# Kernel optimization log

Hardware: AMD Instinct MI355X
Metric: run time of the kernel (lower is better)

Reference implementation:

```python
import jax, jax.numpy as jnp
import numpy as np
from jax import lax

DN = ('NCHW', 'OIHW', 'NCHW')


def _conv_block(x, w, g, b, pool):
    # 3x3 conv (pad 1), BN-inference folded to affine (g, b), ReLU, optional 2x2 maxpool
    x = lax.conv_general_dilated(x, w, (1, 1), 'SAME', dimension_numbers=DN)
    x = jax.nn.relu(x * g[None, :, None, None] + b[None, :, None, None])
    if pool:
        x = lax.reduce_window(x, -jnp.inf, lax.max, (1, 1, 2, 2), (1, 1, 2, 2), 'VALID')
    return x


def _encode(x, w1, g1, b1, w2, g2, b2, w3, g3, b3, w4, g4, b4):
    # Conv64F: pool in blocks 1,2 (84->42->21), no pool in blocks 3,4; then global avg pool
    x = _conv_block(x, w1, g1, b1, True)
    x = _conv_block(x, w2, g2, b2, True)
    x = _conv_block(x, w3, g3, b3, False)
    x = _conv_block(x, w4, g4, b4, False)
    return jnp.mean(x, axis=(2, 3))  # (N, 64)


def setup_inputs() -> dict:
    key = jax.random.key(0)
    ks = jax.random.split(key, 9)
    B, NQ, Way, Shot, C, H, W = 4, 15, 5, 5, 3, 84, 84
    d = {
        'query': jax.random.normal(ks[0], (B, NQ, C, H, W), jnp.float32),
        'support': jax.random.normal(ks[1], (B, Way, Shot, C, H, W), jnp.float32),
        'w1': jax.random.normal(ks[2], (64, 3, 3, 3), jnp.float32) * 0.1,
        'g1': jnp.ones((64,), jnp.float32), 'b1': jnp.zeros((64,), jnp.float32),
        'w2': jax.random.normal(ks[3], (64, 64, 3, 3), jnp.float32) * 0.05,
        'g2': jnp.ones((64,), jnp.float32), 'b2': jnp.zeros((64,), jnp.float32),
        'w3': jax.random.normal(ks[4], (64, 64, 3, 3), jnp.float32) * 0.05,
        'g3': jnp.ones((64,), jnp.float32), 'b3': jnp.zeros((64,), jnp.float32),
        'w4': jax.random.normal(ks[5], (64, 64, 3, 3), jnp.float32) * 0.05,
        'g4': jnp.ones((64,), jnp.float32), 'b4': jnp.zeros((64,), jnp.float32),
        'fc1_w': jax.random.normal(ks[6], (64, 64), jnp.float32) * 0.1,
        'fc1_b': jnp.zeros((64,), jnp.float32),
        'fc2_w': jax.random.normal(ks[7], (32, 64), jnp.float32) * 0.1,
        'fc2_b': jnp.zeros((32,), jnp.float32),
        'fc3_w': jax.random.normal(ks[8], (1, 32), jnp.float32) * 0.1,
        'fc3_b': jnp.zeros((1,), jnp.float32),
    }
    return d


def reference(query, support, w1, g1, b1, w2, g2, b2, w3, g3, b3, w4, g4, b4,
              fc1_w, fc1_b, fc2_w, fc2_b, fc3_w, fc3_b):
    B, NQ, C, H, W = query.shape
    _, Way, Shot = support.shape[:3]
    enc = lambda x: _encode(x, w1, g1, b1, w2, g2, b2, w3, g3, b3, w4, g4, b4)
    q_emb = enc(query.reshape(-1, C, H, W)).reshape(B, NQ, 64)
    s_emb = enc(support.reshape(-1, C, H, W)).reshape(B, Way, Shot, 64)
    # batched pairwise |diff|: (B, NQ, Way, Shot, 64)
    diff = jnp.abs(q_emb[:, :, None, None, :] - s_emb[:, None, :, :, :])
    # relation net (dropout is identity at inference)
    h = jax.nn.relu(jnp.einsum('bqwsd,od->bqwso', diff, fc1_w) + fc1_b)
    h = jax.nn.relu(jnp.einsum('bqwsd,od->bqwso', h, fc2_w) + fc2_b)
    sim = jax.nn.sigmoid(jnp.einsum('bqwsd,od->bqwso', h, fc3_w) + fc3_b)[..., 0]
    scores = jnp.mean(sim, axis=3)  # mean over Shot -> (B, NQ, Way)
    return scores.reshape(B * NQ, Way)
```

## Files before the change

kernel.cpp:

```cpp
#include <hip/hip_runtime.h>
#include <math.h>

typedef unsigned short ushort_t;
typedef __attribute__((ext_vector_type(8))) short bf16x8;
typedef __attribute__((ext_vector_type(16))) float f32x16;

__device__ __forceinline__ ushort_t f2bf(float f) {
    unsigned u = __float_as_uint(f);
    u += 0x7fffu + ((u >> 16) & 1u);
    return (ushort_t)(u >> 16);
}
__device__ __forceinline__ float bf2f(ushort_t h) {
    return __uint_as_float(((unsigned)h) << 16);
}

template <int HP>
__device__ __forceinline__ void zero_halo(ushort_t* buf, int n, int t, int nthr)
{
    const size_t PSTR = (size_t)160 * HP * HP * 32;
    constexpr int W = HP - 2;
    constexpr int NB = 2 * HP + 2 * W;
    for (int j = t; j < 2 * NB; j += nthr) {
        const int pl = j / NB, i = j % NB;
        int yy, xx;
        if (i < HP)            { yy = 0;            xx = i; }
        else if (i < 2 * HP)   { yy = HP - 1;       xx = i - HP; }
        else if (i < 2*HP + W) { yy = i - 2*HP + 1; xx = 0; }
        else                   { yy = i - 2*HP - W + 1; xx = HP - 1; }
        uint4* p = (uint4*)(buf + pl * PSTR +
                            ((size_t)n * HP * HP + yy * HP + xx) * 32);
        const uint4 z = make_uint4(0u, 0u, 0u, 0u);
        p[0] = z; p[1] = z;
    }
}

__global__ __launch_bounds__(256) void prep_k(
    const float* __restrict__ q, const float* __restrict__ s,
    const float* __restrict__ w1, const float* __restrict__ w2,
    const float* __restrict__ w3, const float* __restrict__ w4,
    ushort_t* __restrict__ p0, ushort_t* __restrict__ pw1,
    ushort_t* __restrict__ pw234,
    ushort_t* __restrict__ P1, ushort_t* __restrict__ P2,
    ushort_t* __restrict__ P3, float* __restrict__ embv)
{
    const int b = blockIdx.x, t = threadIdx.x;
    if (b < 160) {
        const int n = b;
        const float* src; int nn;
        if (n < 60) { src = q; nn = n; } else { src = s; nn = n - 60; }
        const float* img = src + (size_t)nn * 3 * 7056;
        for (int px = t; px < 7396; px += 256) {
            const int y = px / 86, x = px % 86;
            uint4 v = make_uint4(0u, 0u, 0u, 0u);
            if (y >= 1 && y <= 84 && x >= 1 && x <= 84) {
                const int o = (y - 1) * 84 + (x - 1);
                const unsigned c0 = f2bf(img[o]);
                const unsigned c1 = f2bf(img[7056 + o]);
                const unsigned c2 = f2bf(img[14112 + o]);
                v.x = c0 | (c1 << 16);
                v.y = c2;
            }
            *(uint4*)(p0 + ((size_t)n * 7396 + px) * 8) = v;
        }
    } else if (b < 167) {
        const int bw = b - 160;
        if (bw == 0) {
            for (int idx = t; idx < 5120; idx += 256) {
                const int sl = idx >> 10, rem = idx & 1023;
                const int co = rem >> 4, c = rem & 15;
                const int h = c >> 3, e = c & 7, tap = 2 * sl + h;
                float v = 0.f;
                if (tap < 9 && e < 3) v = w1[co * 27 + e * 9 + tap];
                pw1[idx] = f2bf(v);
            }
        } else {
            const int l = (bw - 1) >> 1, pass = (bw - 1) & 1;
            const float* w = (l == 0) ? w2 : (l == 1) ? w3 : w4;
            ushort_t* dst = pw234 + l * 36864 + pass * 18432;
            for (int idx = t; idx < 18432; idx += 256) {
                const int c  = idx & 7;
                const int co = (idx >> 3) & 63;
                const int h  = (idx >> 9) & 1;
                const int kl = (idx >> 10) & 1;
                const int tap = idx >> 11;
                const int ci = pass * 32 + kl * 16 + h * 8 + c;
                dst[idx] = f2bf(w[co * 576 + ci * 9 + tap]);
            }
        }
    } else if (b < 327) {
        const int n = b - 167;
        zero_halo<44>(P1, n, t, 256);
        zero_halo<23>(P2, n, t, 256);
        zero_halo<23>(P3, n, t, 256);
    } else {
        for (int i = t; i < 2560; i += 256)
            ((uint4*)embv)[i] = make_uint4(0u, 0u, 0u, 0u);
    }
}

__global__ __launch_bounds__(256, 2) void conv1_lds_k(
    const ushort_t* __restrict__ p0, const ushort_t* __restrict__ pw1,
    const float* __restrict__ gg, const float* __restrict__ bb,
    ushort_t* __restrict__ outp)
{
    constexpr int ROWB = 86 * 16 + 16;
    constexpr int R = 6;
    constexpr int PXB = 84;
    constexpr size_t PLANE1 = (size_t)160 * 1936 * 32;

    __shared__ __align__(16) char alds[R * ROWB];
    __shared__ __align__(16) char blds[10240];

    const int tid = threadIdx.x, wv = tid >> 6, lane = tid & 63;
    const int l31 = lane & 31, h = lane >> 5;
    const int s = blockIdx.x, n = blockIdx.y;
    const int row0 = 4 * s;

    int abase[3];
#pragma unroll
    for (int t = 0; t < 3; ++t) {
        const int ml = wv * 96 + t * 32 + l31;
        int pp = ml >> 2; if (pp > PXB - 1) pp = PXB - 1;
        const int qd = ml & 3;
        const int p = PXB * s + pp;
        const int pr = p / 42, pc = p % 42;
        const int yl = 2 * (pr - 2 * s) + (qd >> 1);
        const int xl = 2 * pc + (qd & 1);
        abase[t] = yl * ROWB + xl * 16;
    }
    int boff[2];
#pragma unroll
    for (int nt = 0; nt < 2; ++nt) boff[nt] = (nt * 32 + l31) * 32 + h * 16;

    {
        const uint4* src = (const uint4*)(p0 + (size_t)n * 7396 * 8);
        for (int i = tid; i < R * 86; i += 256) {
            const int y = i / 86, x = i - y * 86;
            *(uint4*)(alds + y * ROWB + x * 16) = src[(row0 + y) * 86 + x];
        }
    }
    for (int i = tid; i < 640; i += 256)
        ((uint4*)blds)[i] = ((const uint4*)pw1)[i];

    f32x16 acc[3][2];
#pragma unroll
    for (int t = 0; t < 3; ++t)
#pragma unroll
        for (int nt = 0; nt < 2; ++nt)
#pragma unroll
            for (int r = 0; r < 16; ++r) acc[t][nt][r] = 0.f;

    __syncthreads();

#pragma unroll
    for (int st = 0; st < 5; ++st) {
        int tap = 2 * st + h;
        if (tap > 8) tap = 8;
        const int imm = (tap / 3) * ROWB + (tap % 3) * 16;
        const bf16x8 a0 = *(const bf16x8*)(alds + abase[0] + imm);
        const bf16x8 a1 = *(const bf16x8*)(alds + abase[1] + imm);
        const bf16x8 a2 = *(const bf16x8*)(alds + abase[2] + imm);
#pragma unroll
        for (int nt = 0; nt < 2; ++nt) {
            const bf16x8 b = *(const bf16x8*)(blds + st * 2048 + boff[nt]);
            acc[0][nt] = __builtin_amdgcn_mfma_f32_32x32x16_bf16(
                a0, b, acc[0][nt], 0, 0, 0);
            acc[1][nt] = __builtin_amdgcn_mfma_f32_32x32x16_bf16(
                a1, b, acc[1][nt], 0, 0, 0);
            acc[2][nt] = __builtin_amdgcn_mfma_f32_32x32x16_bf16(
                a2, b, acc[2][nt], 0, 0, 0);
        }
    }

    float gv2[2], bv2[2];
#pragma unroll
    for (int nt = 0; nt < 2; ++nt) {
        gv2[nt] = gg[nt * 32 + l31];
        bv2[nt] = bb[nt * 32 + l31];
    }
#pragma unroll
    for (int t = 0; t < 3; ++t) {
#pragma unroll
        for (int g = 0; g < 4; ++g) {
            const int mbase = wv * 96 + t * 32 + 8 * g + 4 * h;
            const int pp = mbase >> 2;
            if (pp >= PXB) continue;
            const int p = PXB * s + pp;
            const int pr = p / 42, pc = p % 42;
            ushort_t* dpix =
                outp + ((size_t)n * 1936 + (pr + 1) * 44 + (pc + 1)) * 32 + l31;
#pragma unroll
            for (int nt = 0; nt < 2; ++nt) {
                float mx = 0.f;
#pragma unroll
                for (int qd = 0; qd < 4; ++qd)
                    mx = fmaxf(mx, fmaf(acc[t][nt][4 * g + qd], gv2[nt], bv2[nt]));
                dpix[nt * PLANE1] = f2bf(mx);
            }
        }
    }
}

template <int HINP, int POOL, int EPI, int RPB, int WAVES>
__device__ __forceinline__ void conv_body(
    const ushort_t* __restrict__ act, const ushort_t* __restrict__ pkw,
    const float* __restrict__ gg, const float* __restrict__ bb,
    ushort_t* __restrict__ outp)
{
    constexpr int MT   = 2;
    constexpr int NTHR = WAVES * 64;
    constexpr int PXB  = 21 * RPB;
    constexpr int R    = POOL ? 2 * RPB + 2 : RPB + 2;
    constexpr int ROWB = HINP * 80;
    const size_t APLANE = (size_t)160 * HINP * HINP * 32;
    constexpr size_t OPLANE = (size_t)160 * 529 * 32;

    __shared__ __align__(16) char alds[R * ROWB];

    const int tid = threadIdx.x, wv = tid >> 6, lane = tid & 63;
    const int l31 = lane & 31, h = lane >> 5;
    const int s = blockIdx.x, n = blockIdx.y;

    const int row0 = POOL ? 2 * RPB * s : RPB * s;

    int abase[MT];
#pragma unroll
    for (int t = 0; t < MT; ++t) {
        const int ml = wv * (MT * 32) + t * 32 + l31;
        int yl, xl;
        if (POOL) {
            int pp = ml >> 2; if (pp > PXB - 1) pp = PXB - 1;
            int p = PXB * s + pp; if (p > 440) p = 440;
            const int qd = ml & 3;
            yl = 2 * (p / 21 - RPB * s) + (qd >> 1);
            xl = 2 * (p % 21) + (qd & 1);
        } else {
            int pp = ml; if (pp > PXB - 1) pp = PXB - 1;
            int p = PXB * s + pp; if (p > 440) p = 440;
            yl = p / 21 - RPB * s;
            xl = p % 21;
        }
        abase[t] = yl * ROWB + xl * 80 + h * 16;
    }
    int boff[2];
#pragma unroll
    for (int nt = 0; nt < 2; ++nt) boff[nt] = h * 1024 + (nt * 32 + l31) * 16;

    f32x16 acc[MT][2];
#pragma unroll
    for (int t = 0; t < MT; ++t)
#pragma unroll
        for (int nt = 0; nt < 2; ++nt)
#pragma unroll
            for (int r = 0; r < 16; ++r) acc[t][nt][r] = 0.f;

    bf16x8 br[4][2];

#define B_LD(S, SLOT)                                                      \
    {                                                                      \
        br[SLOT][0] = *(const bf16x8*)(bg + (S)*2048 + boff[0]);           \
        br[SLOT][1] = *(const bf16x8*)(bg + (S)*2048 + boff[1]);           \
    }

    for (int ph = 0; ph < 2; ++ph) {
        const char* bg = (const char*)pkw + ph * 36864;
        B_LD(0, 0) B_LD(1, 1) B_LD(2, 2) B_LD(3, 3)

        if (ph) __syncthreads();
        {
            const uint4* src = (const uint4*)(act +
                (ph * APLANE + (size_t)n * HINP * HINP * 32));
            for (int p = tid; p < R * HINP; p += NTHR) {
                const int y = p / HINP, x = p - y * HINP;
                const int row = min(row0 + y, HINP - 1);
                const uint4* sp = src + ((size_t)row * HINP + x) * 4;
                const uint4 c0 = sp[0], c1 = sp[1], c2 = sp[2], c3 = sp[3];
                char* d = alds + y * ROWB + x * 80;
                *(uint4*)(d)      = c0;
                *(uint4*)(d + 16) = c1;
                *(uint4*)(d + 32) = c2;
                *(uint4*)(d + 48) = c3;
            }
        }
        __syncthreads();

#pragma unroll
        for (int st = 0; st < 18; ++st) {
            const int sl = st & 3;
            const int tap = st >> 1, kl = st & 1;
            const int imm = (tap / 3) * ROWB + (tap % 3) * 80 + kl * 32;
            const bf16x8 a0 = *(const bf16x8*)(alds + abase[0] + imm);
            const bf16x8 a1 = *(const bf16x8*)(alds + abase[1] + imm);
            const bf16x8 b0 = br[sl][0];
            const bf16x8 b1 = br[sl][1];
            if (st < 14) B_LD(st + 4, sl)
            acc[0][0] = __builtin_amdgcn_mfma_f32_32x32x16_bf16(
                a0, b0, acc[0][0], 0, 0, 0);
            acc[1][0] = __builtin_amdgcn_mfma_f32_32x32x16_bf16(
                a1, b0, acc[1][0], 0, 0, 0);
            acc[0][1] = __builtin_amdgcn_mfma_f32_32x32x16_bf16(
                a0, b1, acc[0][1], 0, 0, 0);
            acc[1][1] = __builtin_amdgcn_mfma_f32_32x32x16_bf16(
                a1, b1, acc[1][1], 0, 0, 0);
        }
    }
#undef B_LD

    float gv2[2], bv2[2];
#pragma unroll
    for (int nt = 0; nt < 2; ++nt) {
        gv2[nt] = gg[nt * 32 + l31];
        bv2[nt] = bb[nt * 32 + l31];
    }

    if (EPI == 0) {
#pragma unroll
        for (int t = 0; t < MT; ++t) {
#pragma unroll
            for (int g = 0; g < 4; ++g) {
                const int mbase = wv * (MT * 32) + t * 32 + 8 * g + 4 * h;
                const int pp = mbase >> 2;
                const int p_img = PXB * s + pp;
                if (pp >= PXB || p_img >= 441) continue;
                const int py = p_img / 21, px = p_img % 21;
                ushort_t* dpix = outp +
                    ((size_t)n * 529 + (py + 1) * 23 + (px + 1)) * 32 + l31;
#pragma unroll
                for (int nt = 0; nt < 2; ++nt) {
                    float mx = 0.f;
#pragma unroll
                    for (int qd = 0; qd < 4; ++qd)
                        mx = fmaxf(mx,
                                   fmaf(acc[t][nt][4 * g + qd], gv2[nt], bv2[nt]));
                    dpix[nt * OPLANE] = f2bf(mx);
                }
            }
        }
    } else if (EPI == 1) {
#pragma unroll
        for (int t = 0; t < MT; ++t) {
#pragma unroll
            for (int r = 0; r < 16; ++r) {
                const int mloc = wv * (MT * 32) + t * 32 +
                                 (r & 3) + 8 * (r >> 2) + 4 * h;
                const int m_img = PXB * s + mloc;
                if (mloc >= PXB || m_img >= 441) continue;
                const int y = m_img / 21, x = m_img % 21;
#pragma unroll
                for (int nt = 0; nt < 2; ++nt) {
                    const float v =
                        fmaxf(fmaf(acc[t][nt][r], gv2[nt], bv2[nt]), 0.f);
                    outp[nt * OPLANE +
                         ((size_t)n * 529 + (y + 1) * 23 + (x + 1)) * 32 + l31] =
                        f2bf(v);
                }
            }
        }
    } else {
        float* embf = (float*)outp;
#pragma unroll
        for (int nt = 0; nt < 2; ++nt) {
            float sum = 0.f;
#pragma unroll
            for (int t = 0; t < MT; ++t) {
#pragma unroll
                for (int r = 0; r < 16; ++r) {
                    const int mloc = wv * (MT * 32) + t * 32 +
                                     (r & 3) + 8 * (r >> 2) + 4 * h;
                    const int m_img = PXB * s + mloc;
                    if (mloc < PXB && m_img < 441)
                        sum += fmaxf(fmaf(acc[t][nt][r], gv2[nt], bv2[nt]), 0.f);
                }
            }
            atomicAdd(&embf[(size_t)n * 64 + nt * 32 + l31],
                      sum * (1.f / 441.f));
        }
    }
}

__global__ __launch_bounds__(256, 4) void conv2_k(
    const ushort_t* __restrict__ act, const ushort_t* __restrict__ pkw,
    const float* __restrict__ gg, const float* __restrict__ bb,
    ushort_t* __restrict__ outp)
{ conv_body<44, 1, 0, 3, 4>(act, pkw, gg, bb, outp); }

__global__ __launch_bounds__(128, 3) void conv3_k(
    const ushort_t* __restrict__ act, const ushort_t* __restrict__ pkw,
    const float* __restrict__ gg, const float* __restrict__ bb,
    ushort_t* __restrict__ outp)
{ conv_body<23, 0, 1, 6, 2>(act, pkw, gg, bb, outp); }

__global__ __launch_bounds__(128, 3) void conv4_k(
    const ushort_t* __restrict__ act, const ushort_t* __restrict__ pkw,
    const float* __restrict__ gg, const float* __restrict__ bb,
    ushort_t* __restrict__ outp)
{ conv_body<23, 0, 2, 6, 2>(act, pkw, gg, bb, outp); }

__global__ __launch_bounds__(64) void relation_k(
    const float* __restrict__ emb,
    const float* __restrict__ fc1w, const float* __restrict__ fc1b,
    const float* __restrict__ fc2w, const float* __restrict__ fc2b,
    const float* __restrict__ fc3w, const float* __restrict__ fc3b,
    float* __restrict__ out)
{
    const int idx = blockIdx.x;
    const int w = idx % 5;
    const int bq = idx / 5;
    const int b = bq / 15;
    const int t = threadIdx.x;

    __shared__ float dif[64], h1v[64], h2v[32];
    const float qv = emb[(size_t)bq * 64 + t];

    float ssum = 0.f;
    for (int s = 0; s < 5; ++s) {
        const int simg = 60 + ((b * 5 + w) * 5 + s);
        __syncthreads();
        dif[t] = fabsf(qv - emb[(size_t)simg * 64 + t]);
        __syncthreads();
        float a = fc1b[t];
        for (int d = 0; d < 64; ++d) a = fmaf(fc1w[t * 64 + d], dif[d], a);
        a = fmaxf(a, 0.f);
        __syncthreads();
        h1v[t] = a;
        __syncthreads();
        if (t < 32) {
            float h = fc2b[t];
            for (int d = 0; d < 64; ++d) h = fmaf(fc2w[t * 64 + d], h1v[d], h);
            h2v[t] = fmaxf(h, 0.f);
        }
        __syncthreads();
        float p = (t < 32) ? fc3w[t] * h2v[t] : 0.f;
#pragma unroll
        for (int off = 32; off > 0; off >>= 1) p += __shfl_down(p, off);
        if (t == 0) {
            const float z = p + fc3b[0];
            ssum += 1.f / (1.f + expf(-z));
        }
    }
    if (t == 0) out[idx] = ssum * 0.2f;
}

extern "C" void kernel_launch(void* const* d_in, const int* in_sizes, int n_in,
                              void* d_out, int out_size, void* d_ws, size_t ws_size,
                              hipStream_t stream)
{
    const float* q    = (const float*)d_in[0];
    const float* s    = (const float*)d_in[1];
    const float* w1   = (const float*)d_in[2];
    const float* g1   = (const float*)d_in[3];
    const float* b1p  = (const float*)d_in[4];
    const float* w2   = (const float*)d_in[5];
    const float* g2   = (const float*)d_in[6];
    const float* b2p  = (const float*)d_in[7];
    const float* w3   = (const float*)d_in[8];
    const float* g3   = (const float*)d_in[9];
    const float* b3p  = (const float*)d_in[10];
    const float* w4   = (const float*)d_in[11];
    const float* g4   = (const float*)d_in[12];
    const float* b4p  = (const float*)d_in[13];
    const float* fc1w = (const float*)d_in[14];
    const float* fc1b = (const float*)d_in[15];
    const float* fc2w = (const float*)d_in[16];
    const float* fc2b = (const float*)d_in[17];
    const float* fc3w = (const float*)d_in[18];
    const float* fc3b = (const float*)d_in[19];
    float* out = (float*)d_out;

    char* ws = (char*)d_ws;
    ushort_t* P0    = (ushort_t*)(ws + 0);
    ushort_t* P1    = (ushort_t*)(ws + 18933760);
    ushort_t* P2    = (ushort_t*)(ws + 58583040);
    ushort_t* P3    = (ushort_t*)(ws + 69416960);
    float*    embv  = (float*)   (ws + 80250880);
    ushort_t* pw1   = (ushort_t*)(ws + 80291840);
    ushort_t* pw234 = (ushort_t*)(ws + 80302080);

    prep_k<<<dim3(328), 256, 0, stream>>>(q, s, w1, w2, w3, w4,
                                          P0, pw1, pw234, P1, P2, P3, embv);

    conv1_lds_k<<<dim3(21, 160), 256, 0, stream>>>(P0, pw1, g1, b1p, P1);

    conv2_k<<<dim3(7, 160), 256, 0, stream>>>(P1, pw234, g2, b2p, P2);
    conv3_k<<<dim3(4, 160), 128, 0, stream>>>(P2, pw234 + 36864, g3, b3p, P3);
    conv4_k<<<dim3(4, 160), 128, 0, stream>>>(
        P3, pw234 + 2 * 36864, g4, b4p, (ushort_t*)embv);

    relation_k<<<dim3(300), 64, 0, stream>>>(
        embv, fc1w, fc1b, fc2w, fc2b, fc3w, fc3b, out);
}
```

Measured before the change: 115.4 us.

## Fuse conv3 and conv4 into one per-image kernel keeping intermediate in LDS

Replaces the separate conv3 and conv4 launches with a single kernel that processes one whole 21x21 image per 512-thread block. The conv3 output, with a zeroed halo, stays in shared memory and feeds conv4 directly, so the P3 global buffer, its halo zeroing, and one launch are removed. The cost is that only 160 blocks of 8 waves are launched, down from 640 smaller blocks per layer, and each block holds about 100KB of LDS, which limits how many blocks fit on a CU and lowers parallelism.

```diff
diff --git a/kernel.cpp b/kernel.cpp
--- a/kernel.cpp
+++ b/kernel.cpp
@@ -41,7 +41,7 @@
     ushort_t* __restrict__ p0, ushort_t* __restrict__ pw1,
     ushort_t* __restrict__ pw234,
     ushort_t* __restrict__ P1, ushort_t* __restrict__ P2,
-    ushort_t* __restrict__ P3, float* __restrict__ embv)
+    float* __restrict__ embv)
 {
     const int b = blockIdx.x, t = threadIdx.x;
     if (b < 160) {
@@ -91,7 +91,6 @@
         const int n = b - 167;
         zero_halo<44>(P1, n, t, 256);
         zero_halo<23>(P2, n, t, 256);
-        zero_halo<23>(P3, n, t, 256);
     } else {
         for (int i = t; i < 2560; i += 256)
             ((uint4*)embv)[i] = make_uint4(0u, 0u, 0u, 0u);
@@ -201,16 +200,15 @@
     }
 }
 
-template <int HINP, int POOL, int EPI, int RPB, int WAVES>
-__device__ __forceinline__ void conv_body(
+__global__ __launch_bounds__(256, 4) void conv2_k(
     const ushort_t* __restrict__ act, const ushort_t* __restrict__ pkw,
     const float* __restrict__ gg, const float* __restrict__ bb,
     ushort_t* __restrict__ outp)
 {
-    constexpr int MT   = 2;
+    constexpr int HINP = 44, RPB = 3, WAVES = 4, MT = 2;
     constexpr int NTHR = WAVES * 64;
     constexpr int PXB  = 21 * RPB;
-    constexpr int R    = POOL ? 2 * RPB + 2 : RPB + 2;
+    constexpr int R    = 2 * RPB + 2;
     constexpr int ROWB = HINP * 80;
     const size_t APLANE = (size_t)160 * HINP * HINP * 32;
     constexpr size_t OPLANE = (size_t)160 * 529 * 32;
@@ -220,26 +218,17 @@
     const int tid = threadIdx.x, wv = tid >> 6, lane = tid & 63;
     const int l31 = lane & 31, h = lane >> 5;
     const int s = blockIdx.x, n = blockIdx.y;
-
-    const int row0 = POOL ? 2 * RPB * s : RPB * s;
+    const int row0 = 2 * RPB * s;
 
     int abase[MT];
 #pragma unroll
     for (int t = 0; t < MT; ++t) {
         const int ml = wv * (MT * 32) + t * 32 + l31;
-        int yl, xl;
-        if (POOL) {
-            int pp = ml >> 2; if (pp > PXB - 1) pp = PXB - 1;
-            int p = PXB * s + pp; if (p > 440) p = 440;
-            const int qd = ml & 3;
-            yl = 2 * (p / 21 - RPB * s) + (qd >> 1);
-            xl = 2 * (p % 21) + (qd & 1);
-        } else {
-            int pp = ml; if (pp > PXB - 1) pp = PXB - 1;
-            int p = PXB * s + pp; if (p > 440) p = 440;
-            yl = p / 21 - RPB * s;
-            xl = p % 21;
-        }
+        int pp = ml >> 2; if (pp > PXB - 1) pp = PXB - 1;
+        int p = PXB * s + pp; if (p > 440) p = 440;
+        const int qd = ml & 3;
+        const int yl = 2 * (p / 21 - RPB * s) + (qd >> 1);
+        const int xl = 2 * (p % 21) + (qd & 1);
         abase[t] = yl * ROWB + xl * 80 + h * 16;
     }
     int boff[2];
@@ -312,89 +301,215 @@
         gv2[nt] = gg[nt * 32 + l31];
         bv2[nt] = bb[nt * 32 + l31];
     }
-
-    if (EPI == 0) {
-#pragma unroll
-        for (int t = 0; t < MT; ++t) {
-#pragma unroll
-            for (int g = 0; g < 4; ++g) {
-                const int mbase = wv * (MT * 32) + t * 32 + 8 * g + 4 * h;
-                const int pp = mbase >> 2;
-                const int p_img = PXB * s + pp;
-                if (pp >= PXB || p_img >= 441) continue;
-                const int py = p_img / 21, px = p_img % 21;
-                ushort_t* dpix = outp +
-                    ((size_t)n * 529 + (py + 1) * 23 + (px + 1)) * 32 + l31;
-#pragma unroll
-                for (int nt = 0; nt < 2; ++nt) {
-                    float mx = 0.f;
-#pragma unroll
-                    for (int qd = 0; qd < 4; ++qd)
-                        mx = fmaxf(mx,
-                                   fmaf(acc[t][nt][4 * g + qd], gv2[nt], bv2[nt]));
-                    dpix[nt * OPLANE] = f2bf(mx);
-                }
-            }
-        }
-    } else if (EPI == 1) {
-#pragma unroll
-        for (int t = 0; t < MT; ++t) {
+#pragma unroll
+    for (int t = 0; t < MT; ++t) {
+#pragma unroll
+        for (int g = 0; g < 4; ++g) {
+            const int mbase = wv * (MT * 32) + t * 32 + 8 * g + 4 * h;
+            const int pp = mbase >> 2;
+            const int p_img = PXB * s + pp;
+            if (pp >= PXB || p_img >= 441) continue;
+            const int py = p_img / 21, px = p_img % 21;
+            ushort_t* dpix = outp +
+                ((size_t)n * 529 + (py + 1) * 23 + (px + 1)) * 32 + l31;
+#pragma unroll
+            for (int nt = 0; nt < 2; ++nt) {
+                float mx = 0.f;
+#pragma unroll
+                for (int qd = 0; qd < 4; ++qd)
+                    mx = fmaxf(mx,
+                               fmaf(acc[t][nt][4 * g + qd], gv2[nt], bv2[nt]));
+                dpix[nt * OPLANE] = f2bf(mx);
+            }
+        }
+    }
+}
+
+__global__ __launch_bounds__(512, 2) void conv34_k(
+    const ushort_t* __restrict__ P2, const ushort_t* __restrict__ pkw3,
+    const ushort_t* __restrict__ pkw4,
+    const float* __restrict__ g3, const float* __restrict__ b3,
+    const float* __restrict__ g4, const float* __restrict__ b4,
+    float* __restrict__ embv)
+{
+    constexpr int ROWB = 23 * 80;
+    constexpr int PLB  = 23 * ROWB;
+    const size_t APLANE = (size_t)160 * 529 * 32;
+
+    __shared__ __align__(16) char alds[PLB];
+    __shared__ __align__(16) char mid[2 * PLB];
+
+    const int tid = threadIdx.x, wv = tid >> 6, lane = tid & 63;
+    const int l31 = lane & 31, h = lane >> 5;
+    const int n = blockIdx.x;
+
+    int abase[2];
+#pragma unroll
+    for (int t = 0; t < 2; ++t) {
+        int ml = wv * 64 + t * 32 + l31;
+        if (ml > 440) ml = 440;
+        abase[t] = (ml / 21) * ROWB + (ml % 21) * 80 + h * 16;
+    }
+    int boff[2];
+#pragma unroll
+    for (int nt = 0; nt < 2; ++nt) boff[nt] = h * 1024 + (nt * 32 + l31) * 16;
+
+    f32x16 acc[2][2];
+#pragma unroll
+    for (int t = 0; t < 2; ++t)
+#pragma unroll
+        for (int nt = 0; nt < 2; ++nt)
+#pragma unroll
+            for (int r = 0; r < 16; ++r) acc[t][nt][r] = 0.f;
+
+    bf16x8 br[4][2];
+
+#define B_LD(S, SLOT)                                                      \
+    {                                                                      \
+        br[SLOT][0] = *(const bf16x8*)(bg + (S)*2048 + boff[0]);           \
+        br[SLOT][1] = *(const bf16x8*)(bg + (S)*2048 + boff[1]);           \
+    }
+
+    for (int ph = 0; ph < 2; ++ph) {
+        const char* bg = (const char*)pkw3 + ph * 36864;
+        B_LD(0, 0) B_LD(1, 1) B_LD(2, 2) B_LD(3, 3)
+
+        if (ph) __syncthreads();
+        {
+            const uint4* src = (const uint4*)(P2 + ph * APLANE +
+                                              (size_t)n * 529 * 32);
+            for (int p = tid; p < 529; p += 512) {
+                const int y = p / 23, x = p - y * 23;
+                const uint4* sp = src + (size_t)p * 4;
+                const uint4 c0 = sp[0], c1 = sp[1], c2 = sp[2], c3 = sp[3];
+                char* d = alds + y * ROWB + x * 80;
+                *(uint4*)(d)      = c0;
+                *(uint4*)(d + 16) = c1;
+                *(uint4*)(d + 32) = c2;
+                *(uint4*)(d + 48) = c3;
+            }
+        }
+        __syncthreads();
+
+#pragma unroll
+        for (int st = 0; st < 18; ++st) {
+            const int sl = st & 3;
+            const int tap = st >> 1, kl = st & 1;
+            const int imm = (tap / 3) * ROWB + (tap % 3) * 80 + kl * 32;
+            const bf16x8 a0 = *(const bf16x8*)(alds + abase[0] + imm);
+            const bf16x8 a1 = *(const bf16x8*)(alds + abase[1] + imm);
+            const bf16x8 b0 = br[sl][0];
+            const bf16x8 b1 = br[sl][1];
+            if (st < 14) B_LD(st + 4, sl)
+            acc[0][0] = __builtin_amdgcn_mfma_f32_32x32x16_bf16(
+                a0, b0, acc[0][0], 0, 0, 0);
+            acc[1][0] = __builtin_amdgcn_mfma_f32_32x32x16_bf16(
+                a1, b0, acc[1][0], 0, 0, 0);
+            acc[0][1] = __builtin_amdgcn_mfma_f32_32x32x16_bf16(
+                a0, b1, acc[0][1], 0, 0, 0);
+            acc[1][1] = __builtin_amdgcn_mfma_f32_32x32x16_bf16(
+                a1, b1, acc[1][1], 0, 0, 0);
+        }
+    }
+
+    {
+        float gv2[2], bv2[2];
+#pragma unroll
+        for (int nt = 0; nt < 2; ++nt) {
+            gv2[nt] = g3[nt * 32 + l31];
+            bv2[nt] = b3[nt * 32 + l31];
+        }
+        for (int j = tid; j < 176; j += 512) {
+            const int pl = j / 88, i = j % 88;
+            int yy, xx;
+            if (i < 23)       { yy = 0;          xx = i; }
+            else if (i < 46)  { yy = 22;         xx = i - 23; }
+            else if (i < 67)  { yy = i - 46 + 1; xx = 0; }
+            else              { yy = i - 67 + 1; xx = 22; }
+            char* d = mid + pl * PLB + yy * ROWB + xx * 80;
+            const uint4 z = make_uint4(0u, 0u, 0u, 0u);
+            *(uint4*)(d)      = z;
+            *(uint4*)(d + 16) = z;
+            *(uint4*)(d + 32) = z;
+            *(uint4*)(d + 48) = z;
+        }
+#pragma unroll
+        for (int t = 0; t < 2; ++t) {
 #pragma unroll
             for (int r = 0; r < 16; ++r) {
-                const int mloc = wv * (MT * 32) + t * 32 +
-                                 (r & 3) + 8 * (r >> 2) + 4 * h;
-                const int m_img = PXB * s + mloc;
-                if (mloc >= PXB || m_img >= 441) continue;
-                const int y = m_img / 21, x = m_img % 21;
+                const int mloc = wv * 64 + t * 32 + (r & 3) + 8 * (r >> 2) + 4 * h;
+                if (mloc >= 441) continue;
+                const int y = mloc / 21, x = mloc % 21;
 #pragma unroll
                 for (int nt = 0; nt < 2; ++nt) {
                     const float v =
                         fmaxf(fmaf(acc[t][nt][r], gv2[nt], bv2[nt]), 0.f);
-                    outp[nt * OPLANE +
-                         ((size_t)n * 529 + (y + 1) * 23 + (x + 1)) * 32 + l31] =
-                        f2bf(v);
+                    *(ushort_t*)(mid + nt * PLB + (y + 1) * ROWB +
+                                 (x + 1) * 80 + l31 * 2) = f2bf(v);
                 }
             }
         }
-    } else {
-        float* embf = (float*)outp;
+    }
+    __syncthreads();
+
+#pragma unroll
+    for (int t = 0; t < 2; ++t)
+#pragma unroll
+        for (int nt = 0; nt < 2; ++nt)
+#pragma unroll
+            for (int r = 0; r < 16; ++r) acc[t][nt][r] = 0.f;
+
+    for (int ph = 0; ph < 2; ++ph) {
+        const char* bg = (const char*)pkw4 + ph * 36864;
+        const char* am = mid + ph * PLB;
+        B_LD(0, 0) B_LD(1, 1) B_LD(2, 2) B_LD(3, 3)
+#pragma unroll
+        for (int st = 0; st < 18; ++st) {
+            const int sl = st & 3;
+            const int tap = st >> 1, kl = st & 1;
+            const int imm = (tap / 3) * ROWB + (tap % 3) * 80 + kl * 32;
+            const bf16x8 a0 = *(const bf16x8*)(am + abase[0] + imm);
+            const bf16x8 a1 = *(const bf16x8*)(am + abase[1] + imm);
+            const bf16x8 b0 = br[sl][0];
+            const bf16x8 b1 = br[sl][1];
+            if (st < 14) B_LD(st + 4, sl)
+            acc[0][0] = __builtin_amdgcn_mfma_f32_32x32x16_bf16(
+                a0, b0, acc[0][0], 0, 0, 0);
+            acc[1][0] = __builtin_amdgcn_mfma_f32_32x32x16_bf16(
+                a1, b0, acc[1][0], 0, 0, 0);
+            acc[0][1] = __builtin_amdgcn_mfma_f32_32x32x16_bf16(
+                a0, b1, acc[0][1], 0, 0, 0);
+            acc[1][1] = __builtin_amdgcn_mfma_f32_32x32x16_bf16(
+                a1, b1, acc[1][1], 0, 0, 0);
+        }
+    }
+#undef B_LD
+
+    {
+        float gv2[2], bv2[2];
+#pragma unroll
+        for (int nt = 0; nt < 2; ++nt) {
+            gv2[nt] = g4[nt * 32 + l31];
+            bv2[nt] = b4[nt * 32 + l31];
+        }
 #pragma unroll
         for (int nt = 0; nt < 2; ++nt) {
             float sum = 0.f;
 #pragma unroll
-            for (int t = 0; t < MT; ++t) {
+            for (int t = 0; t < 2; ++t) {
 #pragma unroll
                 for (int r = 0; r < 16; ++r) {
-                    const int mloc = wv * (MT * 32) + t * 32 +
+                    const int mloc = wv * 64 + t * 32 +
                                      (r & 3) + 8 * (r >> 2) + 4 * h;
-                    const int m_img = PXB * s + mloc;
-                    if (mloc < PXB && m_img < 441)
+                    if (mloc < 441)
                         sum += fmaxf(fmaf(acc[t][nt][r], gv2[nt], bv2[nt]), 0.f);
                 }
             }
-            atomicAdd(&embf[(size_t)n * 64 + nt * 32 + l31],
+            atomicAdd(&embv[(size_t)n * 64 + nt * 32 + l31],
                       sum * (1.f / 441.f));
         }
     }
 }
-
-__global__ __launch_bounds__(256, 4) void conv2_k(
-    const ushort_t* __restrict__ act, const ushort_t* __restrict__ pkw,
-    const float* __restrict__ gg, const float* __restrict__ bb,
-    ushort_t* __restrict__ outp)
-{ conv_body<44, 1, 0, 3, 4>(act, pkw, gg, bb, outp); }
-
-__global__ __launch_bounds__(128, 3) void conv3_k(
-    const ushort_t* __restrict__ act, const ushort_t* __restrict__ pkw,
-    const float* __restrict__ gg, const float* __restrict__ bb,
-    ushort_t* __restrict__ outp)
-{ conv_body<23, 0, 1, 6, 2>(act, pkw, gg, bb, outp); }
-
-__global__ __launch_bounds__(128, 3) void conv4_k(
-    const ushort_t* __restrict__ act, const ushort_t* __restrict__ pkw,
-    const float* __restrict__ gg, const float* __restrict__ bb,
-    ushort_t* __restrict__ outp)
-{ conv_body<23, 0, 2, 6, 2>(act, pkw, gg, bb, outp); }
 
 __global__ __launch_bounds__(64) void relation_k(
     const float* __restrict__ emb,
@@ -471,20 +586,19 @@
     ushort_t* P0    = (ushort_t*)(ws + 0);
     ushort_t* P1    = (ushort_t*)(ws + 18933760);
     ushort_t* P2    = (ushort_t*)(ws + 58583040);
-    ushort_t* P3    = (ushort_t*)(ws + 69416960);
-    float*    embv  = (float*)   (ws + 80250880);
-    ushort_t* pw1   = (ushort_t*)(ws + 80291840);
-    ushort_t* pw234 = (ushort_t*)(ws + 80302080);
+    float*    embv  = (float*)   (ws + 69416960);
+    ushort_t* pw1   = (ushort_t*)(ws + 69457920);
+    ushort_t* pw234 = (ushort_t*)(ws + 69468160);
 
     prep_k<<<dim3(328), 256, 0, stream>>>(q, s, w1, w2, w3, w4,
-                                          P0, pw1, pw234, P1, P2, P3, embv);
+                                          P0, pw1, pw234, P1, P2, embv);
 
     conv1_lds_k<<<dim3(21, 160), 256, 0, stream>>>(P0, pw1, g1, b1p, P1);
 
     conv2_k<<<dim3(7, 160), 256, 0, stream>>>(P1, pw234, g2, b2p, P2);
-    conv3_k<<<dim3(4, 160), 128, 0, stream>>>(P2, pw234 + 36864, g3, b3p, P3);
-    conv4_k<<<dim3(4, 160), 128, 0, stream>>>(
-        P3, pw234 + 2 * 36864, g4, b4p, (ushort_t*)embv);
+
+    conv34_k<<<dim3(160), 512, 0, stream>>>(
+        P2, pw234 + 36864, pw234 + 2 * 36864, g3, b3p, g4, b4p, embv);
 
     relation_k<<<dim3(300), 64, 0, stream>>>(
         embv, fc1w, fc1b, fc2w, fc2b, fc3w, fc3b, out);
```

Result: faster. 109.3 us, median of 2 (-5.3%).
